# Optimization experiments

Hardware: AMD Instinct MI355X
Metric: run time of the kernel (lower is better)

Reference implementation:

```python
import jax, jax.numpy as jnp
import numpy as np
from math import log2

B, N, H, D, HID, BLK = 4, 4096, 16, 64, 1024, 128
THETA = 10000.0
SCALE = D ** -0.5
ATTN_EPS = 1e-8
LN_EPS = 1e-5


def setup_inputs() -> dict:
    key = jax.random.key(0)
    ks = jax.random.split(key, 3)
    return {
        "hidden_states": jax.random.normal(ks[0], (B, N, HID), jnp.float32),
        "ln_gamma": jnp.ones((HID,), jnp.float32),
        "ln_beta": jnp.zeros((HID,), jnp.float32),
        "w_qkv": jax.random.normal(ks[1], (HID, 3 * H * D), jnp.float32) * 0.02,
        "w_out": jax.random.normal(ks[2], (H * D, HID), jnp.float32) * 0.02,
        "b_out": jnp.zeros((HID,), jnp.float32),
    }


def _rotary_freqs(n):
    # faithful to source: 1.0 / (theta ** arange(0,dim,2) / dim)  (note precedence)
    exps = jnp.arange(0, D, 2, dtype=jnp.float32)[: D // 2]
    inv = 1.0 / (THETA ** exps / D)
    f = jnp.arange(n, dtype=jnp.float32)[:, None] * inv[None, :]  # (n, D/2)
    return jnp.repeat(f, 2, axis=-1)  # (n, D), each freq duplicated pairwise


def _apply_rotary(freqs, t):
    cos, sin = jnp.cos(freqs), jnp.sin(freqs)  # (n, D) broadcast over (bh, n, D)
    x = t.reshape(*t.shape[:-1], D // 2, 2)
    rot = jnp.stack((-x[..., 1], x[..., 0]), axis=-1).reshape(t.shape)
    return t * cos + rot * sin


def _flip_pairs(t):
    # flip every adjacent pair along axis 1
    s = t.shape
    t = t.reshape(s[0], s[1] // 2, 2, *s[2:])
    return t[:, :, ::-1].reshape(s)


def _coarsen(q, k, v):
    pair = lambda t: t.reshape(t.shape[0], -1, 2, D)
    return pair(q).mean(2), pair(k).mean(2), pair(v).sum(2)


def _block_attn(q, k, v):
    # q,k,v: (bh, nblk, z, d); unnormalized softmax numerator + denominator
    S = jnp.einsum('bnid,bnjd->bnij', q, k)
    S = S - S.max(-1, keepdims=True)
    A = jnp.exp(S)
    y = jnp.einsum('bnij,bnjd->bnid', A, v)
    return y.reshape(y.shape[0], -1, D), A.sum(-1).reshape(A.shape[0], -1)


def _forward(hidden_states, ln_gamma, ln_beta, w_qkv, w_out, b_out):
    # LayerNorm
    mu = hidden_states.mean(-1, keepdims=True)
    var = hidden_states.var(-1, keepdims=True)
    x = (hidden_states - mu) / jnp.sqrt(var + LN_EPS) * ln_gamma + ln_beta

    # QKV projection, split heads -> (B*H, N, D)
    qkv = x @ w_qkv
    q, k, v = jnp.split(qkv, 3, axis=-1)
    heads = lambda t: t.reshape(B, N, H, D).transpose(0, 2, 1, 3).reshape(B * H, N, D)
    q, k, v = heads(q), heads(k), heads(v)

    q = q * SCALE
    freqs = _rotary_freqs(N)
    q = _apply_rotary(freqs, q)
    k = _apply_rotary(freqs, k)

    num_levels = int(log2(N // BLK)) - 1
    qkvs = [(q, k, v)]
    for _ in range(num_levels):
        qkvs.append(_coarsen(*qkvs[-1]))
    qkvs = [qkvs[0]] + qkvs  # finest level used twice (near + flipped neighbor)

    Ys = []
    n_lv = len(qkvs)
    for ind, (q_, k_, v_) in enumerate(reversed(qkvs)):
        is_last = ind == n_lv - 1
        tb = lambda t: t.reshape(t.shape[0], -1, BLK, D)
        qb, kb, vb = tb(q_), tb(k_), tb(v_)
        if not is_last:
            kb, vb = _flip_pairs(kb), _flip_pairs(vb)
        Ys.append(_block_attn(qb, kb, vb))

    Y, A = Ys[0]
    for ind in range(1, len(Ys)):
        if ind != len(Ys) - 1:
            Y = jnp.repeat(Y, 2, axis=1)
            A = jnp.repeat(A, 2, axis=1)
        Y = Ys[ind][0] + Y
        A = Ys[ind][1] + A

    out = Y / (A + ATTN_EPS)[..., None]
    out = out.reshape(B, H, N, D).transpose(0, 2, 1, 3).reshape(B, N, H * D)
    return out @ w_out + b_out


def reference(hidden_states, ln_gamma, ln_beta, w_qkv, w_out, b_out):
    return _forward(hidden_states, ln_gamma, ln_beta, w_qkv, w_out, b_out)
```

## Files before the change

kernel.cpp:

```cpp
#include <hip/hip_runtime.h>
#include <math.h>

#define NTOK 4096
#define NB 4
#define NH 16
#define HD 64
#define HID 1024
#define BH 64
#define QSCALE 0.125f

typedef unsigned short u16;
typedef unsigned int u32;
typedef __attribute__((ext_vector_type(8))) _Float16 f16x8;
typedef __attribute__((ext_vector_type(8))) short s16x8;
typedef __attribute__((ext_vector_type(4))) float f32x4;
#define MFMA_F16(a, b, c) __builtin_amdgcn_mfma_f32_16x16x32_f16(a, b, c, 0, 0, 0)
#define MFMA_BF16(a, b, c) __builtin_amdgcn_mfma_f32_16x16x32_bf16(a, b, c, 0, 0, 0)
#define GLDS16(gptr, lptr)                                                          \
  __builtin_amdgcn_global_load_lds(                                                \
      (const __attribute__((address_space(1))) void*)(gptr),                       \
      (__attribute__((address_space(3))) void*)(lptr), 16, 0, 0)
#define VMCNT0() asm volatile("s_waitcnt vmcnt(0)" ::: "memory")
#define VMCNT4() asm volatile("s_waitcnt vmcnt(4)" ::: "memory")
#define SCHED_FENCE() __builtin_amdgcn_sched_barrier(0)

__device__ __forceinline__ float bf2f(u32 u) {
  union { u32 i; float f; } x; x.i = u << 16; return x.f;
}
__device__ __forceinline__ u32 f2bf(float f) {
  union { float f; u32 i; } x; x.f = f;
  return (x.i + 0x7fffu + ((x.i >> 16) & 1u)) >> 16;
}
__device__ __forceinline__ u32 pk2(float a, float b) {
  return f2bf(a) | (f2bf(b) << 16);
}
__device__ __forceinline__ u32 pkh2(float a, float b) {
  _Float16 ha = (_Float16)a, hb = (_Float16)b;
  u16 x, y;
  __builtin_memcpy(&x, &ha, 2);
  __builtin_memcpy(&y, &hb, 2);
  return (u32)x | ((u32)y << 16);
}
__device__ __forceinline__ u16 f2h(float a) {
  _Float16 h = (_Float16)a;
  u16 x;
  __builtin_memcpy(&x, &h, 2);
  return x;
}
__device__ __forceinline__ void up8(uint4 a, float* f) {
  f[0] = bf2f(a.x & 0xffffu); f[1] = bf2f(a.x >> 16);
  f[2] = bf2f(a.y & 0xffffu); f[3] = bf2f(a.y >> 16);
  f[4] = bf2f(a.z & 0xffffu); f[5] = bf2f(a.z >> 16);
  f[6] = bf2f(a.w & 0xffffu); f[7] = bf2f(a.w >> 16);
}
__device__ __forceinline__ void up8h(uint4 a, float* f) {
  union { uint4 u; _Float16 h[8]; } x;
  x.u = a;
#pragma unroll
  for (int c = 0; c < 8; ++c) f[c] = (float)x.h[c];
}
__device__ __forceinline__ void up4h(uint2 a, float* f) {
  union { uint2 u; _Float16 h[4]; } x;
  x.u = a;
#pragma unroll
  for (int c = 0; c < 4; ++c) f[c] = (float)x.h[c];
}

__global__ void fill_kernel(float* __restrict__ out, int n, float v) {
  int i = blockIdx.x * 256 + threadIdx.x;
  if (i < n) out[i] = v;
}

__global__ void rope_table_kernel(float* __restrict__ ct, float* __restrict__ st) {
  int idx = blockIdx.x * 256 + threadIdx.x;
  if (idx >= NTOK * 32) return;
  int n = idx >> 5, i = idx & 31;
  float t = powf(10000.0f, (float)(2 * i));
  float inv = 1.0f / (t / 64.0f);
  float f = (float)n * inv;
  ct[idx] = cosf(f);
  st[idx] = sinf(f);
}

__global__ __launch_bounds__(256) void ln_f16_kernel(const float* __restrict__ in,
                                                     const float* __restrict__ gm,
                                                     const float* __restrict__ bt,
                                                     u16* __restrict__ out) {
  __shared__ float sh[8];
  int row = blockIdx.x, t = threadIdx.x;
  float4 x = ((const float4*)(in + (size_t)row * HID))[t];
  float s1 = x.x + x.y + x.z + x.w;
  float s2 = x.x * x.x + x.y * x.y + x.z * x.z + x.w * x.w;
#pragma unroll
  for (int o = 32; o > 0; o >>= 1) {
    s1 += __shfl_down(s1, o, 64);
    s2 += __shfl_down(s2, o, 64);
  }
  if ((t & 63) == 0) { sh[t >> 6] = s1; sh[4 + (t >> 6)] = s2; }
  __syncthreads();
  float S1 = sh[0] + sh[1] + sh[2] + sh[3];
  float S2 = sh[4] + sh[5] + sh[6] + sh[7];
  float mu = S1 * (1.0f / HID);
  float var = S2 * (1.0f / HID) - mu * mu;
  float rstd = 1.0f / sqrtf(var + 1e-5f);
  float4 g = ((const float4*)gm)[t], b = ((const float4*)bt)[t];
  float o0 = (x.x - mu) * rstd * g.x + b.x;
  float o1 = (x.y - mu) * rstd * g.y + b.y;
  float o2 = (x.z - mu) * rstd * g.z + b.z;
  float o3 = (x.w - mu) * rstd * g.w + b.w;
  *(uint2*)&out[(size_t)row * HID + t * 4] = make_uint2(pkh2(o0, o1), pkh2(o2, o3));
}

__global__ __launch_bounds__(256) void prep_w_kernel(const float* __restrict__ w,
                                                     u16* __restrict__ wt, int N) {
  __shared__ float T[64][65];
  int t = threadIdx.x;
  int n0 = blockIdx.x * 64, k0 = blockIdx.y * 64;
  {
    int k = t >> 2, nc = (t & 3) * 16;
    const float* src = w + (size_t)(k0 + k) * N + n0 + nc;
#pragma unroll
    for (int i = 0; i < 4; ++i) {
      float4 x = *(const float4*)(src + i * 4);
      T[nc + i * 4 + 0][k] = x.x;
      T[nc + i * 4 + 1][k] = x.y;
      T[nc + i * 4 + 2][k] = x.z;
      T[nc + i * 4 + 3][k] = x.w;
    }
  }
  __syncthreads();
  {
    int n = t >> 2, kc = (t & 3) * 16;
    u32 pk[8];
#pragma unroll
    for (int j = 0; j < 8; ++j) pk[j] = pkh2(T[n][kc + 2 * j], T[n][kc + 2 * j + 1]);
    size_t dst = (size_t)(n0 + n) * 1024 + k0 + kc;
    *(uint4*)&wt[dst] = make_uint4(pk[0], pk[1], pk[2], pk[3]);
    *(uint4*)&wt[dst + 8] = make_uint4(pk[4], pk[5], pk[6], pk[7]);
  }
}

__global__ __launch_bounds__(256) void transpose_v_kernel(const u16* __restrict__ vf,
                                                          u16* __restrict__ vt) {
  __shared__ u16 T[64][72];
  int bh = blockIdx.y, tok0 = blockIdx.x * 64;
  int t = threadIdx.x;
  {
    int tk = t >> 2, d0 = (t & 3) * 16;
    const u16* src = vf + ((size_t)bh * NTOK + tok0 + tk) * HD + d0;
    *(uint4*)&T[tk][d0] = *(const uint4*)src;
    *(uint4*)&T[tk][d0 + 8] = *(const uint4*)(src + 8);
  }
  __syncthreads();
  {
    int dv = t >> 2, k0 = (t & 3) * 16;
    union { u16 v[16]; uint4 q[2]; } o;
#pragma unroll
    for (int i = 0; i < 16; ++i) o.v[i] = T[k0 + i][dv];
    u16* dst = vt + ((size_t)bh * HD + dv) * NTOK + tok0 + k0;
    *(uint4*)dst = o.q[0];
    *(uint4*)(dst + 8) = o.q[1];
  }
}

template <int MODE>
__global__ __launch_bounds__(256) void gemm_f16_kernel(
    const u16* __restrict__ At, const u16* __restrict__ Bt,
    u16* __restrict__ qd, u16* __restrict__ kd, u16* __restrict__ vd,
    const float* __restrict__ ct, const float* __restrict__ st,
    const float* __restrict__ bias, float* __restrict__ C, int nxb) {
  constexpr int BUF = 128 * 32;
  __shared__ __align__(16) u16 As[3 * BUF], Bs[3 * BUF];
  const int t = threadIdx.x;
  const int nwg = gridDim.x;
  const int bid = blockIdx.x;
  const int wid = (bid & 7) * (nwg >> 3) + (bid >> 3);
  const int m0 = (wid / nxb) * 128, n0 = (wid % nxb) * 128;
  const int l = t & 63, w = t >> 6;
  const int wm = w & 1, wn = w >> 1;
  const int lr = l & 15;
  const int kgs = (((l >> 4) ^ ((lr >> 1) & 3))) * 8;

  const int schunk = (l & 3) ^ ((l >> 3) & 3);
  const u16* gA = At + (size_t)(m0 + w * 32 + (l >> 2)) * 1024 + schunk * 8;
  const u16* gB = Bt + (size_t)(n0 + w * 32 + (l >> 2)) * 1024 + schunk * 8;
  const int wbase = (w * 32) * 32;

  f32x4 zero4 = {0.f, 0.f, 0.f, 0.f};
  f32x4 acc[4][4];
#pragma unroll
  for (int mf = 0; mf < 4; ++mf)
#pragma unroll
    for (int nf = 0; nf < 4; ++nf) acc[mf][nf] = zero4;

  GLDS16(gA, &As[wbase]);
  GLDS16(gA + (size_t)16 * 1024, &As[wbase + 16 * 32]);
  GLDS16(gB, &Bs[wbase]);
  GLDS16(gB + (size_t)16 * 1024, &Bs[wbase + 16 * 32]);
  GLDS16(gA + 32, &As[BUF + wbase]);
  GLDS16(gA + 32 + (size_t)16 * 1024, &As[BUF + wbase + 16 * 32]);
  GLDS16(gB + 32, &Bs[BUF + wbase]);
  GLDS16(gB + 32 + (size_t)16 * 1024, &Bs[BUF + wbase + 16 * 32]);
  VMCNT4();
  __builtin_amdgcn_s_barrier();
  SCHED_FENCE();

  int cur = 0;
  for (int step = 0; step < 32; ++step) {
    int nx2 = cur + 2; if (nx2 >= 3) nx2 -= 3;
    if (step + 2 < 32) {
      int k2 = (step + 2) * 32;
      GLDS16(gA + k2, &As[nx2 * BUF + wbase]);
      GLDS16(gA + k2 + (size_t)16 * 1024, &As[nx2 * BUF + wbase + 16 * 32]);
      GLDS16(gB + k2, &Bs[nx2 * BUF + wbase]);
      GLDS16(gB + k2 + (size_t)16 * 1024, &Bs[nx2 * BUF + wbase + 16 * 32]);
    }
    {
      const int cb = cur * BUF;
      f16x8 af[4];
#pragma unroll
      for (int mf = 0; mf < 4; ++mf)
        af[mf] = *(const f16x8*)&As[cb + (wm * 64 + mf * 16 + lr) * 32 + kgs];
#pragma unroll
      for (int nf = 0; nf < 4; ++nf) {
        f16x8 bf = *(const f16x8*)&Bs[cb + (wn * 64 + nf * 16 + lr) * 32 + kgs];
#pragma unroll
        for (int mf = 0; mf < 4; ++mf) acc[mf][nf] = MFMA_F16(af[mf], bf, acc[mf][nf]);
      }
    }
    if (step + 1 < 32) {
      SCHED_FENCE();
      if (step + 2 < 32) VMCNT4();
      else               VMCNT0();
      __builtin_amdgcn_s_barrier();
      SCHED_FENCE();
    }
    cur = cur + 1; if (cur >= 3) cur -= 3;
  }

  if (MODE == 0) {
#pragma unroll
    for (int nf = 0; nf < 4; ++nf) {
      int col = n0 + wn * 64 + nf * 16 + (l & 15);
      int which = col >> 10;
      int rem = col & 1023;
      int h = rem >> 6, d = rem & 63;
      int fi = d >> 1;
      float sc = (which == 0) ? QSCALE : 1.0f;
#pragma unroll
      for (int mf = 0; mf < 4; ++mf) {
#pragma unroll
        for (int r = 0; r < 4; ++r) {
          int row = m0 + wm * 64 + mf * 16 + (l >> 4) * 4 + r;
          int bbo = row >> 12, n = row & 4095;
          size_t idx = ((size_t)(bbo * NH + h) * NTOK + n) * HD + d;
          float val = acc[mf][nf][r];
          if (which == 2) {
            vd[idx] = f2h(val);
          } else {
            float par = __shfl_xor(val, 1);
            float cc = ct[n * 32 + fi], ss = st[n * 32 + fi];
            float a0 = val * sc, a1 = par * sc;
            float o = (d & 1) ? fmaf(a0, cc, a1 * ss) : fmaf(a0, cc, -(a1 * ss));
            ((which == 0) ? qd : kd)[idx] = (u16)f2bf(o);
          }
        }
      }
    }
  } else {
#pragma unroll
    for (int nf = 0; nf < 4; ++nf) {
      int col = n0 + wn * 64 + nf * 16 + (l & 15);
      float bl_ = bias[col];
#pragma unroll
      for (int mf = 0; mf < 4; ++mf) {
#pragma unroll
        for (int r = 0; r < 4; ++r) {
          int row = m0 + wm * 64 + mf * 16 + (l >> 4) * 4 + r;
          C[(size_t)row * 1024 + col] = acc[mf][nf][r] + bl_;
        }
      }
    }
  }
}

#define KP 72
#define VP 136
#define PP 136
template <int LV, int FINE>
__global__ __launch_bounds__(256, 2) void attn_mfma_kernel(
    const u16* __restrict__ qg, const u16* __restrict__ kgl, const u16* __restrict__ vtg,
    u16* __restrict__ yl, float* __restrict__ al) {
  constexpr int R = 1 << LV;
  constexpr float QKSC = 1.0f / (float)R;
  __shared__ __align__(16) u16 Ks[128 * KP];
  __shared__ __align__(16) u16 Vt[64 * VP];
  __shared__ __align__(16) u16 Ps[128 * PP];
  const int t = threadIdx.x;
  const int blk = blockIdx.x, bh = blockIdx.y;
  const int l = t & 63, w = t >> 6;
  const int lr = l & 15, lg = l >> 4;
  const int nl = NTOK >> LV;
  const size_t bbase = (size_t)bh * NTOK;

  s16x8 aq[2][2];
#pragma unroll
  for (int qf = 0; qf < 2; ++qf)
#pragma unroll
    for (int ks = 0; ks < 2; ++ks) {
      int qrow = blk * 128 + w * 32 + qf * 16 + lr;
      const u16* src = qg + (bbase + ((size_t)qrow << LV)) * HD + ks * 32 + lg * 8;
      if (LV == 0) {
        aq[qf][ks] = *(const s16x8*)src;
      } else {
        float s[8] = {};
#pragma unroll
        for (int ss = 0; ss < R; ++ss) {
          uint4 a = *(const uint4*)(src + (size_t)ss * HD);
          float f[8];
          up8(a, f);
#pragma unroll
          for (int c = 0; c < 8; ++c) s[c] += f[c];
        }
        union { uint4 u; s16x8 v; } cv;
        cv.u = make_uint4(pk2(s[0] * QKSC, s[1] * QKSC), pk2(s[2] * QKSC, s[3] * QKSC),
                          pk2(s[4] * QKSC, s[5] * QKSC), pk2(s[6] * QKSC, s[7] * QKSC));
        aq[qf][ks] = cv.v;
      }
    }

  f32x4 zero4 = {0.f, 0.f, 0.f, 0.f};
  f32x4 accYT[4][2];
  float asum[2] = {0.f, 0.f};
#pragma unroll
  for (int dvf = 0; dvf < 4; ++dvf)
#pragma unroll
    for (int qf = 0; qf < 2; ++qf) accYT[dvf][qf] = zero4;

  const int npass = FINE ? 2 : 1;
  for (int pass = 0; pass < npass; ++pass) {
    const int kblk = (pass == 0) ? (blk ^ 1) : blk;
    __syncthreads();
#pragma unroll
    for (int it = 0; it < 2; ++it) {
      int kk = it * 64 + (t >> 2), dq = (t & 3) * 16;
      const u16* src = kgl + (bbase + (((size_t)kblk * 128 + kk) << LV)) * HD + dq;
      if (LV == 0) {
        *(uint4*)&Ks[kk * KP + dq] = *(const uint4*)src;
        *(uint4*)&Ks[kk * KP + dq + 8] = *(const uint4*)(src + 8);
      } else {
        float s[16] = {};
#pragma unroll
        for (int ss = 0; ss < R; ++ss) {
          float f[8];
          up8(*(const uint4*)(src + (size_t)ss * HD), f);
#pragma unroll
          for (int c = 0; c < 8; ++c) s[c] += f[c];
          up8(*(const uint4*)(src + (size_t)ss * HD + 8), f);
#pragma unroll
          for (int c = 0; c < 8; ++c) s[8 + c] += f[c];
        }
        u32 pk[8];
#pragma unroll
        for (int j = 0; j < 8; ++j) pk[j] = pk2(s[2 * j] * QKSC, s[2 * j + 1] * QKSC);
        *(uint4*)&Ks[kk * KP + dq] = make_uint4(pk[0], pk[1], pk[2], pk[3]);
        *(uint4*)&Ks[kk * KP + dq + 8] = make_uint4(pk[4], pk[5], pk[6], pk[7]);
      }
    }
    {
      int dv = t >> 2, j0 = (t & 3) * 32;
      const u16* src = vtg + ((size_t)bh * HD + dv) * NTOK +
                       (((size_t)(kblk * 128 + j0)) << LV);
      if (LV == 0) {
#pragma unroll
        for (int c = 0; c < 4; ++c)
          *(uint4*)&Vt[dv * VP + j0 + c * 8] = *(const uint4*)(src + c * 8);
      } else {
        float acc[32];
#pragma unroll
        for (int j = 0; j < 32; ++j) acc[j] = 0.f;
#pragma unroll
        for (int c = 0; c < 4 * R; ++c) {
          float f[8];
          up8h(*(const uint4*)(src + c * 8), f);
#pragma unroll
          for (int e = 0; e < 8; ++e) acc[(c * 8 + e) >> LV] += f[e];
        }
#pragma unroll
        for (int j = 0; j < 32; j += 8) {
          uint4 pkv;
          pkv.x = pkh2(acc[j + 0], acc[j + 1]);
          pkv.y = pkh2(acc[j + 2], acc[j + 3]);
          pkv.z = pkh2(acc[j + 4], acc[j + 5]);
          pkv.w = pkh2(acc[j + 6], acc[j + 7]);
          *(uint4*)&Vt[dv * VP + j0 + j] = pkv;
        }
      }
    }
    __syncthreads();
    f32x4 accST[8][2];
#pragma unroll
    for (int kf = 0; kf < 8; ++kf)
#pragma unroll
      for (int qf = 0; qf < 2; ++qf) accST[kf][qf] = zero4;
#pragma unroll
    for (int kf = 0; kf < 8; ++kf)
#pragma unroll
      for (int ks = 0; ks < 2; ++ks) {
        s16x8 ak = *(const s16x8*)&Ks[(kf * 16 + lr) * KP + ks * 32 + lg * 8];
        accST[kf][0] = MFMA_BF16(ak, aq[0][ks], accST[kf][0]);
        accST[kf][1] = MFMA_BF16(ak, aq[1][ks], accST[kf][1]);
      }
#pragma unroll
    for (int qf = 0; qf < 2; ++qf) {
      float m = accST[0][qf][0];
#pragma unroll
      for (int kf = 0; kf < 8; ++kf)
#pragma unroll
        for (int r = 0; r < 4; ++r) m = fmaxf(m, accST[kf][qf][r]);
      m = fmaxf(m, __shfl_xor(m, 16));
      m = fmaxf(m, __shfl_xor(m, 32));
      float s = 0.f;
#pragma unroll
      for (int kf = 0; kf < 8; ++kf) {
#pragma unroll
        for (int r = 0; r < 4; ++r) {
          float e = __expf(accST[kf][qf][r] - m);
          accST[kf][qf][r] = e;
          s += e;
        }
      }
      s += __shfl_xor(s, 16);
      s += __shfl_xor(s, 32);
      asum[qf] += s;
#pragma unroll
      for (int kf = 0; kf < 8; ++kf) {
        uint2 pw;
        pw.x = pkh2(accST[kf][qf][0], accST[kf][qf][1]);
        pw.y = pkh2(accST[kf][qf][2], accST[kf][qf][3]);
        *(uint2*)&Ps[(w * 32 + qf * 16 + lr) * PP + kf * 16 + lg * 4] = pw;
      }
    }
#pragma unroll
    for (int ks4 = 0; ks4 < 4; ++ks4) {
      f16x8 pf[2];
#pragma unroll
      for (int qf = 0; qf < 2; ++qf)
        pf[qf] = *(const f16x8*)&Ps[(w * 32 + qf * 16 + lr) * PP + ks4 * 32 + lg * 8];
#pragma unroll
      for (int dvf = 0; dvf < 4; ++dvf) {
        f16x8 vf = *(const f16x8*)&Vt[(dvf * 16 + lr) * VP + ks4 * 32 + lg * 8];
        accYT[dvf][0] = MFMA_F16(vf, pf[0], accYT[dvf][0]);
        accYT[dvf][1] = MFMA_F16(vf, pf[1], accYT[dvf][1]);
      }
    }
  }
#pragma unroll
  for (int qf = 0; qf < 2; ++qf) {
    if (lg == 0)
      al[(size_t)bh * nl + blk * 128 + w * 32 + qf * 16 + lr] = asum[qf];
    int q = blk * 128 + w * 32 + qf * 16 + lr;
#pragma unroll
    for (int dvf = 0; dvf < 4; ++dvf) {
      uint2 yw;
      yw.x = pkh2(accYT[dvf][qf][0], accYT[dvf][qf][1]);
      yw.y = pkh2(accYT[dvf][qf][2], accYT[dvf][qf][3]);
      *(uint2*)&yl[((size_t)bh * nl + q) * HD + dvf * 16 + lg * 4] = yw;
    }
  }
}

__global__ __launch_bounds__(256) void combine_pyr_kernel(
    const u16* __restrict__ Yf, const u16* __restrict__ Y1, const u16* __restrict__ Y2,
    const u16* __restrict__ Y3, const u16* __restrict__ Y4,
    const float* __restrict__ Af, const float* __restrict__ A1, const float* __restrict__ A2,
    const float* __restrict__ A3, const float* __restrict__ A4, u16* __restrict__ out) {
  int row = blockIdx.x, t = threadIdx.x;
  int b = row >> 12, tok = row & 4095;
  int h = t >> 4, d = (t & 15) * 4;
  int bh = b * NH + h;
  float a = Af[(size_t)bh * 4096 + tok] + A1[(size_t)bh * 2048 + (tok >> 1)] +
            A2[(size_t)bh * 1024 + (tok >> 2)] + A3[(size_t)bh * 512 + (tok >> 3)] +
            A4[(size_t)bh * 256 + (tok >> 4)] + 1e-8f;
  float y[4] = {0.f, 0.f, 0.f, 0.f}, f[4];
  up4h(*(const uint2*)&Yf[((size_t)bh * 4096 + tok) * HD + d], f);
#pragma unroll
  for (int c = 0; c < 4; ++c) y[c] += f[c];
  up4h(*(const uint2*)&Y1[((size_t)bh * 2048 + (tok >> 1)) * HD + d], f);
#pragma unroll
  for (int c = 0; c < 4; ++c) y[c] += f[c];
  up4h(*(const uint2*)&Y2[((size_t)bh * 1024 + (tok >> 2)) * HD + d], f);
#pragma unroll
  for (int c = 0; c < 4; ++c) y[c] += f[c];
  up4h(*(const uint2*)&Y3[((size_t)bh * 512 + (tok >> 3)) * HD + d], f);
#pragma unroll
  for (int c = 0; c < 4; ++c) y[c] += f[c];
  up4h(*(const uint2*)&Y4[((size_t)bh * 256 + (tok >> 4)) * HD + d], f);
#pragma unroll
  for (int c = 0; c < 4; ++c) y[c] += f[c];
  float inv = 1.0f / a;
  *(uint2*)&out[(size_t)row * HID + t * 4] =
      make_uint2(pkh2(y[0] * inv, y[1] * inv), pkh2(y[2] * inv, y[3] * inv));
}

extern "C" void kernel_launch(void* const* d_in, const int* in_sizes, int n_in,
                              void* d_out, int out_size, void* d_ws, size_t ws_size,
                              hipStream_t stream) {
  (void)in_sizes; (void)n_in;
  const float* hs = (const float*)d_in[0];
  const float* gm = (const float*)d_in[1];
  const float* bt = (const float*)d_in[2];
  const float* wqkv = (const float*)d_in[3];
  const float* wout = (const float*)d_in[4];
  const float* bout = (const float*)d_in[5];
  float* out = (float*)d_out;

  const size_t MB = 1024ull * 1024ull;
  unsigned char* base = (unsigned char*)d_ws;
  const size_t need = 233 * MB;
  if (ws_size < need) {
    fill_kernel<<<(out_size + 255) / 256, 256, 0, stream>>>(out, out_size,
                                                            1000.0f + (float)(ws_size >> 20));
    return;
  }

  u16* Qf = (u16*)(base);
  u16* Kf = (u16*)(base + 32 * MB);
  u16* Vf = (u16*)(base + 64 * MB);
  u16* Yf = (u16*)(base + 96 * MB);
  u16* VT = (u16*)(base + 128 * MB);
  u16* Y1 = (u16*)(base + 160 * MB);
  u16* Y2 = (u16*)(base + 176 * MB);
  u16* Y3 = (u16*)(base + 184 * MB);
  u16* Y4 = (u16*)(base + 188 * MB);
  float* AACC = (float*)(base + 190 * MB);
  float* A1 = AACC + (size_t)BH * 4096;
  float* A2 = A1 + (size_t)BH * 2048;
  float* A3 = A2 + (size_t)BH * 1024;
  float* A4 = A3 + (size_t)BH * 512;
  u16* WQT = (u16*)(base + 192 * MB);
  u16* WOT = (u16*)(base + 198 * MB);
  float* CT = (float*)(base + 200 * MB);
  float* ST = CT + NTOK * 32;
  u16* ALN = (u16*)(base + 201 * MB);
  u16* ATT = (u16*)(base);

  rope_table_kernel<<<(NTOK * 32 + 255) / 256, 256, 0, stream>>>(CT, ST);
  ln_f16_kernel<<<NB * NTOK, 256, 0, stream>>>(hs, gm, bt, ALN);
  prep_w_kernel<<<dim3(48, 16), 256, 0, stream>>>(wqkv, WQT, 3072);
  prep_w_kernel<<<dim3(16, 16), 256, 0, stream>>>(wout, WOT, 1024);

  gemm_f16_kernel<0><<<3072, 256, 0, stream>>>(
      ALN, WQT, Qf, Kf, Vf, CT, ST, nullptr, nullptr, 24);
  transpose_v_kernel<<<dim3(NTOK / 64, BH), 256, 0, stream>>>(Vf, VT);

  attn_mfma_kernel<0, 1><<<dim3(32, BH), 256, 0, stream>>>(Qf, Kf, VT, Yf, AACC);
  attn_mfma_kernel<1, 0><<<dim3(16, BH), 256, 0, stream>>>(Qf, Kf, VT, Y1, A1);
  attn_mfma_kernel<2, 0><<<dim3(8, BH), 256, 0, stream>>>(Qf, Kf, VT, Y2, A2);
  attn_mfma_kernel<3, 0><<<dim3(4, BH), 256, 0, stream>>>(Qf, Kf, VT, Y3, A3);
  attn_mfma_kernel<4, 0><<<dim3(2, BH), 256, 0, stream>>>(Qf, Kf, VT, Y4, A4);

  combine_pyr_kernel<<<NB * NTOK, 256, 0, stream>>>(Yf, Y1, Y2, Y3, Y4,
                                                    AACC, A1, A2, A3, A4, ATT);
  gemm_f16_kernel<1><<<1024, 256, 0, stream>>>(
      ATT, WOT, nullptr, nullptr, nullptr, nullptr, nullptr, bout, out, 8);
}
```

Before: 540.1 us.

## Use 256x256 GEMM tiles with 512 threads and fuse V transpose into epilogue

Replaces the 128x128, 256-thread triple-buffered f16 GEMM with a 256x256, 512-thread double-buffered kernel. It uses K-steps of 64, an XOR-swizzled LDS layout, staging loads interleaved with MFMA groups, and s_setprio around the MFMA bursts. The aim is more operand reuse per LDS byte and less global traffic per FLOP. The QKV epilogue now writes V directly in transposed f16 layout, so the separate transpose kernel and the intermediate V buffer go away. The trade-off is 128KB of LDS per block, which limits occupancy, fewer blocks for the output projection, and strided 8-byte stores for V.

```diff
diff --git a/kernel.cpp b/kernel.cpp
--- a/kernel.cpp
+++ b/kernel.cpp
@@ -21,7 +21,7 @@
       (const __attribute__((address_space(1))) void*)(gptr),                       \
       (__attribute__((address_space(3))) void*)(lptr), 16, 0, 0)
 #define VMCNT0() asm volatile("s_waitcnt vmcnt(0)" ::: "memory")
-#define VMCNT4() asm volatile("s_waitcnt vmcnt(4)" ::: "memory")
+#define VMCNT2() asm volatile("s_waitcnt vmcnt(2)" ::: "memory")
 #define SCHED_FENCE() __builtin_amdgcn_sched_barrier(0)
 
 __device__ __forceinline__ float bf2f(u32 u) {
@@ -140,128 +140,107 @@
   }
 }
 
-__global__ __launch_bounds__(256) void transpose_v_kernel(const u16* __restrict__ vf,
-                                                          u16* __restrict__ vt) {
-  __shared__ u16 T[64][72];
-  int bh = blockIdx.y, tok0 = blockIdx.x * 64;
-  int t = threadIdx.x;
-  {
-    int tk = t >> 2, d0 = (t & 3) * 16;
-    const u16* src = vf + ((size_t)bh * NTOK + tok0 + tk) * HD + d0;
-    *(uint4*)&T[tk][d0] = *(const uint4*)src;
-    *(uint4*)&T[tk][d0 + 8] = *(const uint4*)(src + 8);
-  }
-  __syncthreads();
-  {
-    int dv = t >> 2, k0 = (t & 3) * 16;
-    union { u16 v[16]; uint4 q[2]; } o;
-#pragma unroll
-    for (int i = 0; i < 16; ++i) o.v[i] = T[k0 + i][dv];
-    u16* dst = vt + ((size_t)bh * HD + dv) * NTOK + tok0 + k0;
-    *(uint4*)dst = o.q[0];
-    *(uint4*)(dst + 8) = o.q[1];
-  }
-}
-
 template <int MODE>
-__global__ __launch_bounds__(256) void gemm_f16_kernel(
+__global__ __launch_bounds__(512, 2) void gemm256_kernel(
     const u16* __restrict__ At, const u16* __restrict__ Bt,
-    u16* __restrict__ qd, u16* __restrict__ kd, u16* __restrict__ vd,
+    u16* __restrict__ qd, u16* __restrict__ kd, u16* __restrict__ vtd,
     const float* __restrict__ ct, const float* __restrict__ st,
     const float* __restrict__ bias, float* __restrict__ C, int nxb) {
-  constexpr int BUF = 128 * 32;
-  __shared__ __align__(16) u16 As[3 * BUF], Bs[3 * BUF];
+  __shared__ __align__(16) u16 As[2][256 * 64], Bs[2][256 * 64];
   const int t = threadIdx.x;
-  const int nwg = gridDim.x;
-  const int bid = blockIdx.x;
+  const int nwg = gridDim.x, bid = blockIdx.x;
   const int wid = (bid & 7) * (nwg >> 3) + (bid >> 3);
-  const int m0 = (wid / nxb) * 128, n0 = (wid % nxb) * 128;
+  const int m0 = (wid / nxb) * 256, n0 = (wid % nxb) * 256;
   const int l = t & 63, w = t >> 6;
-  const int wm = w & 1, wn = w >> 1;
-  const int lr = l & 15;
-  const int kgs = (((l >> 4) ^ ((lr >> 1) & 3))) * 8;
-
-  const int schunk = (l & 3) ^ ((l >> 3) & 3);
-  const u16* gA = At + (size_t)(m0 + w * 32 + (l >> 2)) * 1024 + schunk * 8;
-  const u16* gB = Bt + (size_t)(n0 + w * 32 + (l >> 2)) * 1024 + schunk * 8;
-  const int wbase = (w * 32) * 32;
+  const int wm = w >> 2, wn = w & 3;
+  const int lr = l & 15, lg = l >> 4;
+  const int swr = lr & 7;
+
+  const int swz = (l & 7) ^ (l >> 3);
+  const u16* gA = At + (size_t)(m0 + w * 8 + (l >> 3)) * 1024 + swz * 8;
+  const u16* gB = Bt + (size_t)(n0 + w * 8 + (l >> 3)) * 1024 + swz * 8;
+  const int ldst = (w * 8) * 64;
+
+#define STAGE_A(sl, a, kt) GLDS16(gA + (size_t)(a) * 64 * 1024 + (kt) * 64, &As[sl][(a) * 64 * 64 + ldst])
+#define STAGE_B(sl, a, kt) GLDS16(gB + (size_t)(a) * 64 * 1024 + (kt) * 64, &Bs[sl][(a) * 64 * 64 + ldst])
 
   f32x4 zero4 = {0.f, 0.f, 0.f, 0.f};
-  f32x4 acc[4][4];
-#pragma unroll
-  for (int mf = 0; mf < 4; ++mf)
+  f32x4 acc[8][4];
+#pragma unroll
+  for (int mf = 0; mf < 8; ++mf)
 #pragma unroll
     for (int nf = 0; nf < 4; ++nf) acc[mf][nf] = zero4;
 
-  GLDS16(gA, &As[wbase]);
-  GLDS16(gA + (size_t)16 * 1024, &As[wbase + 16 * 32]);
-  GLDS16(gB, &Bs[wbase]);
-  GLDS16(gB + (size_t)16 * 1024, &Bs[wbase + 16 * 32]);
-  GLDS16(gA + 32, &As[BUF + wbase]);
-  GLDS16(gA + 32 + (size_t)16 * 1024, &As[BUF + wbase + 16 * 32]);
-  GLDS16(gB + 32, &Bs[BUF + wbase]);
-  GLDS16(gB + 32 + (size_t)16 * 1024, &Bs[BUF + wbase + 16 * 32]);
-  VMCNT4();
-  __builtin_amdgcn_s_barrier();
-  SCHED_FENCE();
-
-  int cur = 0;
-  for (int step = 0; step < 32; ++step) {
-    int nx2 = cur + 2; if (nx2 >= 3) nx2 -= 3;
-    if (step + 2 < 32) {
-      int k2 = (step + 2) * 32;
-      GLDS16(gA + k2, &As[nx2 * BUF + wbase]);
-      GLDS16(gA + k2 + (size_t)16 * 1024, &As[nx2 * BUF + wbase + 16 * 32]);
-      GLDS16(gB + k2, &Bs[nx2 * BUF + wbase]);
-      GLDS16(gB + k2 + (size_t)16 * 1024, &Bs[nx2 * BUF + wbase + 16 * 32]);
-    }
-    {
-      const int cb = cur * BUF;
-      f16x8 af[4];
-#pragma unroll
-      for (int mf = 0; mf < 4; ++mf)
-        af[mf] = *(const f16x8*)&As[cb + (wm * 64 + mf * 16 + lr) * 32 + kgs];
-#pragma unroll
-      for (int nf = 0; nf < 4; ++nf) {
-        f16x8 bf = *(const f16x8*)&Bs[cb + (wn * 64 + nf * 16 + lr) * 32 + kgs];
-#pragma unroll
-        for (int mf = 0; mf < 4; ++mf) acc[mf][nf] = MFMA_F16(af[mf], bf, acc[mf][nf]);
-      }
-    }
-    if (step + 1 < 32) {
-      SCHED_FENCE();
-      if (step + 2 < 32) VMCNT4();
-      else               VMCNT0();
-      __builtin_amdgcn_s_barrier();
-      SCHED_FENCE();
-    }
-    cur = cur + 1; if (cur >= 3) cur -= 3;
-  }
+#pragma unroll
+  for (int a = 0; a < 4; ++a) { STAGE_A(0, a, 0); STAGE_B(0, a, 0); }
+
+#pragma unroll 2
+  for (int j = 0; j < 16; ++j) {
+    const int slot = j & 1, nsl = slot ^ 1;
+    __builtin_amdgcn_s_barrier();
+    if (j + 1 < 16) { STAGE_A(nsl, 0, j + 1); STAGE_B(nsl, 0, j + 1); }
+    if (j + 1 < 16) VMCNT2();
+    else           VMCNT0();
+    SCHED_FENCE();
+    f16x8 bf[4][2];
+#pragma unroll
+    for (int nf = 0; nf < 4; ++nf)
+#pragma unroll
+      for (int ks = 0; ks < 2; ++ks)
+        bf[nf][ks] = *(const f16x8*)&Bs[slot][(wn * 64 + nf * 16 + lr) * 64 +
+                                             (((ks << 2) + lg) ^ swr) * 8];
+#pragma unroll
+    for (int q = 0; q < 4; ++q) {
+      if (j + 1 < 16 && q < 3) { STAGE_A(nsl, q + 1, j + 1); STAGE_B(nsl, q + 1, j + 1); }
+      f16x8 af[2][2];
+#pragma unroll
+      for (int mm = 0; mm < 2; ++mm)
+#pragma unroll
+        for (int ks = 0; ks < 2; ++ks)
+          af[mm][ks] = *(const f16x8*)&As[slot][(wm * 128 + (2 * q + mm) * 16 + lr) * 64 +
+                                               (((ks << 2) + lg) ^ swr) * 8];
+      __builtin_amdgcn_s_setprio(1);
+#pragma unroll
+      for (int mm = 0; mm < 2; ++mm)
+#pragma unroll
+        for (int nf = 0; nf < 4; ++nf)
+#pragma unroll
+          for (int ks = 0; ks < 2; ++ks)
+            acc[2 * q + mm][nf] = MFMA_F16(af[mm][ks], bf[nf][ks], acc[2 * q + mm][nf]);
+      __builtin_amdgcn_s_setprio(0);
+    }
+  }
+#undef STAGE_A
+#undef STAGE_B
 
   if (MODE == 0) {
 #pragma unroll
     for (int nf = 0; nf < 4; ++nf) {
-      int col = n0 + wn * 64 + nf * 16 + (l & 15);
+      int col = n0 + wn * 64 + nf * 16 + lr;
       int which = col >> 10;
       int rem = col & 1023;
       int h = rem >> 6, d = rem & 63;
       int fi = d >> 1;
       float sc = (which == 0) ? QSCALE : 1.0f;
 #pragma unroll
-      for (int mf = 0; mf < 4; ++mf) {
-#pragma unroll
-        for (int r = 0; r < 4; ++r) {
-          int row = m0 + wm * 64 + mf * 16 + (l >> 4) * 4 + r;
-          int bbo = row >> 12, n = row & 4095;
-          size_t idx = ((size_t)(bbo * NH + h) * NTOK + n) * HD + d;
-          float val = acc[mf][nf][r];
-          if (which == 2) {
-            vd[idx] = f2h(val);
-          } else {
+      for (int mf = 0; mf < 8; ++mf) {
+        int row0 = m0 + wm * 128 + mf * 16 + lg * 4;
+        int bbo = row0 >> 12;
+        int n = row0 & 4095;
+        if (which == 2) {
+          uint2 yw;
+          yw.x = pkh2(acc[mf][nf][0], acc[mf][nf][1]);
+          yw.y = pkh2(acc[mf][nf][2], acc[mf][nf][3]);
+          *(uint2*)&vtd[((size_t)(bbo * NH + h) * HD + d) * NTOK + n] = yw;
+        } else {
+#pragma unroll
+          for (int r = 0; r < 4; ++r) {
+            float val = acc[mf][nf][r];
             float par = __shfl_xor(val, 1);
-            float cc = ct[n * 32 + fi], ss = st[n * 32 + fi];
+            float cc = ct[(n + r) * 32 + fi], ss = st[(n + r) * 32 + fi];
             float a0 = val * sc, a1 = par * sc;
             float o = (d & 1) ? fmaf(a0, cc, a1 * ss) : fmaf(a0, cc, -(a1 * ss));
+            size_t idx = ((size_t)(bbo * NH + h) * NTOK + n + r) * HD + d;
             ((which == 0) ? qd : kd)[idx] = (u16)f2bf(o);
           }
         }
@@ -270,15 +249,14 @@
   } else {
 #pragma unroll
     for (int nf = 0; nf < 4; ++nf) {
-      int col = n0 + wn * 64 + nf * 16 + (l & 15);
+      int col = n0 + wn * 64 + nf * 16 + lr;
       float bl_ = bias[col];
 #pragma unroll
-      for (int mf = 0; mf < 4; ++mf) {
-#pragma unroll
-        for (int r = 0; r < 4; ++r) {
-          int row = m0 + wm * 64 + mf * 16 + (l >> 4) * 4 + r;
-          C[(size_t)row * 1024 + col] = acc[mf][nf][r] + bl_;
-        }
+      for (int mf = 0; mf < 8; ++mf) {
+        int row0 = m0 + wm * 128 + mf * 16 + lg * 4;
+#pragma unroll
+        for (int r = 0; r < 4; ++r)
+          C[(size_t)(row0 + r) * 1024 + col] = acc[mf][nf][r] + bl_;
       }
     }
   }
@@ -526,9 +504,8 @@
 
   u16* Qf = (u16*)(base);
   u16* Kf = (u16*)(base + 32 * MB);
-  u16* Vf = (u16*)(base + 64 * MB);
+  u16* VT = (u16*)(base + 64 * MB);
   u16* Yf = (u16*)(base + 96 * MB);
-  u16* VT = (u16*)(base + 128 * MB);
   u16* Y1 = (u16*)(base + 160 * MB);
   u16* Y2 = (u16*)(base + 176 * MB);
   u16* Y3 = (u16*)(base + 184 * MB);
@@ -550,9 +527,8 @@
   prep_w_kernel<<<dim3(48, 16), 256, 0, stream>>>(wqkv, WQT, 3072);
   prep_w_kernel<<<dim3(16, 16), 256, 0, stream>>>(wout, WOT, 1024);
 
-  gemm_f16_kernel<0><<<3072, 256, 0, stream>>>(
-      ALN, WQT, Qf, Kf, Vf, CT, ST, nullptr, nullptr, 24);
-  transpose_v_kernel<<<dim3(NTOK / 64, BH), 256, 0, stream>>>(Vf, VT);
+  gemm256_kernel<0><<<768, 512, 0, stream>>>(
+      ALN, WQT, Qf, Kf, VT, CT, ST, nullptr, nullptr, 12);
 
   attn_mfma_kernel<0, 1><<<dim3(32, BH), 256, 0, stream>>>(Qf, Kf, VT, Yf, AACC);
   attn_mfma_kernel<1, 0><<<dim3(16, BH), 256, 0, stream>>>(Qf, Kf, VT, Y1, A1);
@@ -562,6 +538,6 @@
 
   combine_pyr_kernel<<<NB * NTOK, 256, 0, stream>>>(Yf, Y1, Y2, Y3, Y4,
                                                     AACC, A1, A2, A3, A4, ATT);
-  gemm_f16_kernel<1><<<1024, 256, 0, stream>>>(
-      ATT, WOT, nullptr, nullptr, nullptr, nullptr, nullptr, bout, out, 8);
-}
+  gemm256_kernel<1><<<256, 512, 0, stream>>>(
+      ATT, WOT, nullptr, nullptr, nullptr, nullptr, nullptr, bout, out, 4);
+}
```

After: 476.0 us. -11.9%, faster.
